# Performance work log

Hardware: AMD Instinct MI355X
Metric: run time of the kernel (lower is better)

## Reference

```python
import jax, jax.numpy as jnp
import numpy as np

B, H, S, D = 4, 16, 4096, 64

def setup_inputs() -> dict:
    key = jax.random.key(0)
    kq, kk, kv, km = jax.random.split(key, 4)
    Q = jax.random.normal(kq, (B, H, S, D), dtype=jnp.float32)
    K = jax.random.normal(kk, (B, H, S, D), dtype=jnp.float32)
    V = jax.random.normal(kv, (B, H, S, D), dtype=jnp.float32)
    mask = jax.random.randint(km, (B, S), 0, 2, dtype=jnp.int32)
    return {"Q": Q, "K": K, "V": V, "mask": mask}

def reference(Q, K, V, mask):
    Q = jax.nn.relu(Q)
    K = jax.nn.relu(K)
    # zero out masked-out key positions: mask [B,S] -> [B,1,S,1]
    m = mask.astype(bool)[:, None, :, None]
    K = jnp.where(m, K, jnp.zeros((), K.dtype))
    # attn_inter = K^T V : [B,H,D,D]
    attn_inter = jnp.einsum('bhsd,bhse->bhde', K, V)
    # attn_weights = Q @ attn_inter : [B,H,S,D]
    attn_weights = jnp.einsum('bhsd,bhde->bhse', Q, attn_inter)
    # norm = Q @ sum_s K : [B,H,S,1]
    k_sum = K.sum(axis=2)  # [B,H,D]
    norm = jnp.einsum('bhsd,bhd->bhs', Q, k_sum)[..., None]
    return attn_weights / norm
```

## Files before the change

### kernel.cpp

```cpp
#include <hip/hip_runtime.h>
#include <hip/hip_bf16.h>

#define SDIM 4096
#define DDIM 64
#define HN   16
#define BH   64
#define NC   16

typedef __attribute__((ext_vector_type(8))) short short8;
typedef __attribute__((ext_vector_type(4))) float f32x4;

static __device__ __forceinline__ unsigned f2bfu(float f) {
    __hip_bfloat16 h = __float2bfloat16(f);
    return (unsigned)*reinterpret_cast<unsigned short*>(&h);
}
static __device__ __forceinline__ short f2bfs(float f) {
    __hip_bfloat16 h = __float2bfloat16(f);
    return *reinterpret_cast<short*>(&h);
}

#define KTPITCH 136

__global__ __launch_bounds__(256, 4) void k1_kv(
    const float* __restrict__ K, const float* __restrict__ V,
    const int* __restrict__ mask,
    float* __restrict__ KVp, float* __restrict__ ksump)
{
    __shared__ __align__(16) char smem[35840];
    char* const KT0 = smem;
    char* const VT0 = smem + 8704;
    char* const KT1 = smem + 17408;
    char* const VT1 = smem + 26112;
    float* const kswork = (float*)(smem + 34816);

    const int tid = threadIdx.x;
    const int w = tid >> 6, l = tid & 63;
    const int a = l & 15, quad = l >> 4;
    const int bh = blockIdx.x >> 4, ch = blockIdx.x & 15;
    const int b  = bh >> 4;
    const long base = (long)bh * SDIM * DDIM;
    const int s0 = ch * 256;

    const int rb  = tid >> 4;
    const int c4  = (tid & 15) << 2;
    const int par = rb & 1;

    f32x4 acc[4];
#pragma unroll
    for (int i = 0; i < 4; ++i) acc[i] = (f32x4){0.f, 0.f, 0.f, 0.f};
    float ks4[4] = {0.f, 0.f, 0.f, 0.f};

    f32x4 kr[4], vr[4];
    float mr[4];
#pragma unroll
    for (int i = 0; i < 4; ++i) {
        const int row = rb + 16 * i;
        kr[i] = *(const f32x4*)(K + base + (long)(s0 + row) * DDIM + c4);
        vr[i] = *(const f32x4*)(V + base + (long)(s0 + row) * DDIM + c4);
        mr[i] = mask[b * SDIM + s0 + row] ? 1.f : 0.f;
    }

    for (int t = 0; t < 4; ++t) {
        char* const KT = (t & 1) ? KT1 : KT0;
        char* const VT = (t & 1) ? VT1 : VT0;

#pragma unroll
        for (int i = 0; i < 4; ++i) {
            const int row = rb + 16 * i;
            const int sp  = row >> 1;
            float kq[4], vq[4];
            kq[0] = fmaxf(kr[i].x, 0.f) * mr[i];
            kq[1] = fmaxf(kr[i].y, 0.f) * mr[i];
            kq[2] = fmaxf(kr[i].z, 0.f) * mr[i];
            kq[3] = fmaxf(kr[i].w, 0.f) * mr[i];
            vq[0] = vr[i].x; vq[1] = vr[i].y; vq[2] = vr[i].z; vq[3] = vr[i].w;
#pragma unroll
            for (int j = 0; j < 4; ++j) ks4[j] += kq[j];
            unsigned ku[4], vu[4];
#pragma unroll
            for (int j = 0; j < 4; ++j) {
                ku[j] = f2bfu(kq[j]);
                vu[j] = f2bfu(vq[j]);
            }
            unsigned kp32[4], vp32[4];
#pragma unroll
            for (int j = 0; j < 4; ++j) {
                const unsigned pk = (unsigned)__shfl_xor((int)ku[j], 16);
                const unsigned pv = (unsigned)__shfl_xor((int)vu[j], 16);
                kp32[j] = par ? (pk | (ku[j] << 16)) : (ku[j] | (pk << 16));
                vp32[j] = par ? (pv | (vu[j] << 16)) : (vu[j] | (pv << 16));
            }
            const int j0 = par * 2;
            *(unsigned*)(KT + (c4 + j0)     * KTPITCH + sp * 4) = kp32[j0];
            *(unsigned*)(KT + (c4 + j0 + 1) * KTPITCH + sp * 4) = kp32[j0 + 1];
            *(unsigned*)(VT + (c4 + j0)     * KTPITCH + sp * 4) = vp32[j0];
            *(unsigned*)(VT + (c4 + j0 + 1) * KTPITCH + sp * 4) = vp32[j0 + 1];
        }

        if (t < 3) {
            const int r0n = s0 + (t + 1) * 64;
#pragma unroll
            for (int i = 0; i < 4; ++i) {
                const int row = rb + 16 * i;
                kr[i] = *(const f32x4*)(K + base + (long)(r0n + row) * DDIM + c4);
                vr[i] = *(const f32x4*)(V + base + (long)(r0n + row) * DDIM + c4);
                mr[i] = mask[b * SDIM + r0n + row] ? 1.f : 0.f;
            }
        }

        __syncthreads();

#pragma unroll
        for (int kh = 0; kh < 2; ++kh) {
            const int sof = kh * 64 + quad * 16;
            short8 af[4];
#pragma unroll
            for (int dt = 0; dt < 4; ++dt) {
                const char* rp = KT + (dt * 16 + a) * KTPITCH + sof;
                const uint2 lo = *(const uint2*)rp;
                const uint2 hi = *(const uint2*)(rp + 8);
                int4 ra; ra.x = lo.x; ra.y = lo.y; ra.z = hi.x; ra.w = hi.y;
                af[dt] = *(short8*)&ra;
            }
            const char* vp = VT + (w * 16 + a) * KTPITCH + sof;
            const uint2 vlo = *(const uint2*)vp;
            const uint2 vhi = *(const uint2*)(vp + 8);
            int4 rb4; rb4.x = vlo.x; rb4.y = vlo.y; rb4.z = vhi.x; rb4.w = vhi.y;
            const short8 bf = *(short8*)&rb4;
#pragma unroll
            for (int dt = 0; dt < 4; ++dt)
                acc[dt] = __builtin_amdgcn_mfma_f32_16x16x32_bf16(
                    af[dt], bf, acc[dt], 0, 0, 0);
        }
    }

#pragma unroll
    for (int j = 0; j < 4; ++j) {
        ks4[j] += __shfl_xor(ks4[j], 16);
        ks4[j] += __shfl_xor(ks4[j], 32);
    }
    __syncthreads();
    float* const kb = (float*)smem;
#pragma unroll
    for (int dt = 0; dt < 4; ++dt)
#pragma unroll
        for (int r = 0; r < 4; ++r) {
            const int d = dt * 16 + quad * 4 + r;
            const int e = w * 16 + a;
            kb[d * 64 + (e ^ (((d >> 3) & 3) << 4))] = acc[dt][r];
        }
    if (l < 16) {
#pragma unroll
        for (int j = 0; j < 4; ++j) kswork[w * 64 + l * 4 + j] = ks4[j];
    }
    __syncthreads();
    float* outp = KVp + ((long)bh * NC + ch) * 4096;
#pragma unroll
    for (int i = 0; i < 16; ++i) {
        const int idx = i * 256 + tid;
        const int d = idx >> 6, e = idx & 63;
        outp[idx] = kb[d * 64 + (e ^ (((d >> 3) & 3) << 4))];
    }
    if (tid < 64)
        ksump[((long)bh * NC + ch) * 64 + tid] =
            kswork[tid] + kswork[64 + tid] + kswork[128 + tid] + kswork[192 + tid];
}

__global__ __launch_bounds__(256) void k2_reduce(
    const float* __restrict__ KVp, const float* __restrict__ ksump,
    float* __restrict__ KV, float* __restrict__ ksum)
{
    const int bh = blockIdx.x >> 2;
    const int qt = blockIdx.x & 3;
    const int tid = threadIdx.x;
#pragma unroll
    for (int i = 0; i < 4; ++i) {
        const int idx = qt * 1024 + i * 256 + tid;
        float v = 0.f;
#pragma unroll
        for (int c = 0; c < NC; ++c) v += KVp[((long)bh * NC + c) * 4096 + idx];
        KV[(long)bh * 4096 + idx] = v;
    }
    if (qt == 0 && tid < 64) {
        float v = 0.f;
#pragma unroll
        for (int c = 0; c < NC; ++c) v += ksump[((long)bh * NC + c) * 64 + tid];
        ksum[bh * 64 + tid] = v;
    }
}

__global__ __launch_bounds__(256, 4) void k3_out(
    const float* __restrict__ Q, const float* __restrict__ KVm,
    const float* __restrict__ ksum, float* __restrict__ out)
{
    __shared__ float cbuf[4][16 * 68];
    const int tid  = threadIdx.x;
    const int w    = tid >> 6;
    const int l    = tid & 63;
    const int r16  = l & 15;
    const int quad = l >> 4;
    const int bh    = blockIdx.x >> 4;
    const int strip = blockIdx.x & 15;

    const float* kvp = KVm + (long)bh * 4096;
    short8 bfrag[2][4];
#pragma unroll
    for (int kh = 0; kh < 2; ++kh)
#pragma unroll
        for (int n = 0; n < 4; ++n) {
            short8 tmp;
#pragma unroll
            for (int j = 0; j < 8; ++j)
                tmp[j] = f2bfs(kvp[(kh * 32 + quad * 8 + j) * 64 + n * 16 + r16]);
            bfrag[kh][n] = tmp;
        }
    float ksv[16];
#pragma unroll
    for (int j = 0; j < 8; ++j) {
        ksv[j]     = ksum[bh * 64 + quad * 8 + j];
        ksv[j + 8] = ksum[bh * 64 + 32 + quad * 8 + j];
    }

    const int rowbase = strip * 256 + w * 64;
    const float* qptr = Q + ((long)bh * SDIM + rowbase + r16) * DDIM + quad * 8;
    float* obase = out + ((long)bh * SDIM + rowbase) * DDIM;
    float* cw = &cbuf[w][0];

    f32x4 a0 = *(const f32x4*)(qptr);
    f32x4 a1 = *(const f32x4*)(qptr + 4);
    f32x4 a2 = *(const f32x4*)(qptr + 32);
    f32x4 a3 = *(const f32x4*)(qptr + 36);

    for (int t = 0; t < 4; ++t) {
        f32x4 b0 = a0, b1 = a1, b2 = a2, b3 = a3;
        if (t < 3) {
            const float* qn = qptr + (t + 1) * 16 * DDIM;
            b0 = *(const f32x4*)(qn);
            b1 = *(const f32x4*)(qn + 4);
            b2 = *(const f32x4*)(qn + 32);
            b3 = *(const f32x4*)(qn + 36);
        }
#pragma unroll
        for (int j = 0; j < 4; ++j) {
            a0[j] = fmaxf(a0[j], 0.f); a1[j] = fmaxf(a1[j], 0.f);
            a2[j] = fmaxf(a2[j], 0.f); a3[j] = fmaxf(a3[j], 0.f);
        }
        float p = 0.f;
#pragma unroll
        for (int j = 0; j < 4; ++j) {
            p = fmaf(a0[j], ksv[j],      p);
            p = fmaf(a1[j], ksv[4 + j],  p);
            p = fmaf(a2[j], ksv[8 + j],  p);
            p = fmaf(a3[j], ksv[12 + j], p);
        }
        p += __shfl_xor(p, 16);
        p += __shfl_xor(p, 32);
        const float inv = __builtin_amdgcn_rcpf(p);

        short8 af0, af1;
#pragma unroll
        for (int j = 0; j < 4; ++j) {
            af0[j]     = f2bfs(a0[j]);
            af0[4 + j] = f2bfs(a1[j]);
            af1[j]     = f2bfs(a2[j]);
            af1[4 + j] = f2bfs(a3[j]);
        }

        f32x4 acc[4];
#pragma unroll
        for (int n = 0; n < 4; ++n) {
            acc[n] = (f32x4){0.f, 0.f, 0.f, 0.f};
            acc[n] = __builtin_amdgcn_mfma_f32_16x16x32_bf16(af0, bfrag[0][n], acc[n], 0, 0, 0);
            acc[n] = __builtin_amdgcn_mfma_f32_16x16x32_bf16(af1, bfrag[1][n], acc[n], 0, 0, 0);
        }

        float invr[4];
#pragma unroll
        for (int r = 0; r < 4; ++r) invr[r] = __shfl(inv, quad * 4 + r);

#pragma unroll
        for (int n = 0; n < 4; ++n)
#pragma unroll
            for (int r = 0; r < 4; ++r)
                cw[(quad * 4 + r) * 68 + n * 16 + r16] = acc[n][r] * invr[r];

        float* ot = obase + (t * 16) * DDIM;
#pragma unroll
        for (int i = 0; i < 4; ++i) {
            f32x4 v = *(const f32x4*)(cw + (i * 4 + quad) * 68 + r16 * 4);
            *(f32x4*)(ot + (i * 4 + quad) * DDIM + r16 * 4) = v;
        }
        a0 = b0; a1 = b1; a2 = b2; a3 = b3;
    }
}

extern "C" void kernel_launch(void* const* d_in, const int* in_sizes, int n_in,
                              void* d_out, int out_size, void* d_ws, size_t ws_size,
                              hipStream_t stream)
{
    const float* Q    = (const float*)d_in[0];
    const float* K    = (const float*)d_in[1];
    const float* V    = (const float*)d_in[2];
    const int*   mask = (const int*)d_in[3];
    float* out = (float*)d_out;

    float* KVp   = out;
    float* ksump = KVp + (long)BH * NC * 4096;
    float* KV    = (float*)d_ws;
    float* ksum  = KV + (long)BH * 4096;

    hipLaunchKernelGGL(k1_kv, dim3(BH * NC), dim3(256), 0, stream,
                       K, V, mask, KVp, ksump);
    hipLaunchKernelGGL(k2_reduce, dim3(BH * 4), dim3(256), 0, stream,
                       KVp, ksump, KV, ksum);
    hipLaunchKernelGGL(k3_out, dim3(BH * 16), dim3(256), 0, stream,
                       Q, KV, ksum, out);
}
```

Before: 67.64 us.

## Split sequence chunk across waves with per-wave full KV tiles and LDS reduction

```diff
diff --git a/kernel.cpp b/kernel.cpp
--- a/kernel.cpp
+++ b/kernel.cpp
@@ -19,120 +19,109 @@
     return *reinterpret_cast<short*>(&h);
 }
 
-#define KTPITCH 136
-
-__global__ __launch_bounds__(256, 4) void k1_kv(
+#define SPITCH 72
+
+__global__ __launch_bounds__(256, 3) void k1_kv(
     const float* __restrict__ K, const float* __restrict__ V,
     const int* __restrict__ mask,
     float* __restrict__ KVp, float* __restrict__ ksump)
 {
-    __shared__ __align__(16) char smem[35840];
-    char* const KT0 = smem;
-    char* const VT0 = smem + 8704;
-    char* const KT1 = smem + 17408;
-    char* const VT1 = smem + 26112;
-    float* const kswork = (float*)(smem + 34816);
-
+    __shared__ __align__(16) char smem[36864];
     const int tid = threadIdx.x;
     const int w = tid >> 6, l = tid & 63;
     const int a = l & 15, quad = l >> 4;
     const int bh = blockIdx.x >> 4, ch = blockIdx.x & 15;
     const int b  = bh >> 4;
     const long base = (long)bh * SDIM * DDIM;
-    const int s0 = ch * 256;
-
-    const int rb  = tid >> 4;
-    const int c4  = (tid & 15) << 2;
-    const int par = rb & 1;
-
-    f32x4 acc[4];
-#pragma unroll
-    for (int i = 0; i < 4; ++i) acc[i] = (f32x4){0.f, 0.f, 0.f, 0.f};
+    const int s0 = ch * 256 + w * 64;
+
+    char* const KT = smem + w * 9216;
+    char* const VT = smem + w * 9216 + 4608;
+    const int par = quad & 1;
+    const int c4  = a << 2;
+
+    f32x4 acc[4][4];
+#pragma unroll
+    for (int i = 0; i < 4; ++i)
+#pragma unroll
+        for (int j = 0; j < 4; ++j) acc[i][j] = (f32x4){0.f, 0.f, 0.f, 0.f};
     float ks4[4] = {0.f, 0.f, 0.f, 0.f};
 
-    f32x4 kr[4], vr[4];
-    float mr[4];
-#pragma unroll
-    for (int i = 0; i < 4; ++i) {
-        const int row = rb + 16 * i;
-        kr[i] = *(const f32x4*)(K + base + (long)(s0 + row) * DDIM + c4);
-        vr[i] = *(const f32x4*)(V + base + (long)(s0 + row) * DDIM + c4);
-        mr[i] = mask[b * SDIM + s0 + row] ? 1.f : 0.f;
-    }
-
-    for (int t = 0; t < 4; ++t) {
-        char* const KT = (t & 1) ? KT1 : KT0;
-        char* const VT = (t & 1) ? VT1 : VT0;
-
-#pragma unroll
-        for (int i = 0; i < 4; ++i) {
-            const int row = rb + 16 * i;
-            const int sp  = row >> 1;
-            float kq[4], vq[4];
-            kq[0] = fmaxf(kr[i].x, 0.f) * mr[i];
-            kq[1] = fmaxf(kr[i].y, 0.f) * mr[i];
-            kq[2] = fmaxf(kr[i].z, 0.f) * mr[i];
-            kq[3] = fmaxf(kr[i].w, 0.f) * mr[i];
-            vq[0] = vr[i].x; vq[1] = vr[i].y; vq[2] = vr[i].z; vq[3] = vr[i].w;
-#pragma unroll
-            for (int j = 0; j < 4; ++j) ks4[j] += kq[j];
+    auto LOADG = [&](int g, f32x4* kr, f32x4* vr, float* mr) {
+#pragma unroll
+        for (int gg = 0; gg < 4; ++gg) {
+            const int row = s0 + g * 16 + gg * 4 + quad;
+            kr[gg] = *(const f32x4*)(K + base + (long)row * DDIM + c4);
+            vr[gg] = *(const f32x4*)(V + base + (long)row * DDIM + c4);
+            mr[gg] = mask[b * SDIM + row] ? 1.f : 0.f;
+        }
+    };
+    auto PACKG = [&](int g, f32x4* kr, f32x4* vr, float* mr) {
+#pragma unroll
+        for (int gg = 0; gg < 4; ++gg) {
+            float kq[4];
+#pragma unroll
+            for (int j = 0; j < 4; ++j) {
+                kq[j] = fmaxf(kr[gg][j], 0.f) * mr[gg];
+                ks4[j] += kq[j];
+            }
             unsigned ku[4], vu[4];
 #pragma unroll
             for (int j = 0; j < 4; ++j) {
                 ku[j] = f2bfu(kq[j]);
-                vu[j] = f2bfu(vq[j]);
+                vu[j] = f2bfu(vr[gg][j]);
             }
-            unsigned kp32[4], vp32[4];
+            const int sp = (g & 1) * 8 + gg * 2 + (quad >> 1);
+            const int j0 = par * 2;
+            unsigned kp[4], vp[4];
 #pragma unroll
             for (int j = 0; j < 4; ++j) {
                 const unsigned pk = (unsigned)__shfl_xor((int)ku[j], 16);
                 const unsigned pv = (unsigned)__shfl_xor((int)vu[j], 16);
-                kp32[j] = par ? (pk | (ku[j] << 16)) : (ku[j] | (pk << 16));
-                vp32[j] = par ? (pv | (vu[j] << 16)) : (vu[j] | (pv << 16));
+                kp[j] = par ? (pk | (ku[j] << 16)) : (ku[j] | (pk << 16));
+                vp[j] = par ? (pv | (vu[j] << 16)) : (vu[j] | (pv << 16));
             }
-            const int j0 = par * 2;
-            *(unsigned*)(KT + (c4 + j0)     * KTPITCH + sp * 4) = kp32[j0];
-            *(unsigned*)(KT + (c4 + j0 + 1) * KTPITCH + sp * 4) = kp32[j0 + 1];
-            *(unsigned*)(VT + (c4 + j0)     * KTPITCH + sp * 4) = vp32[j0];
-            *(unsigned*)(VT + (c4 + j0 + 1) * KTPITCH + sp * 4) = vp32[j0 + 1];
-        }
-
-        if (t < 3) {
-            const int r0n = s0 + (t + 1) * 64;
-#pragma unroll
-            for (int i = 0; i < 4; ++i) {
-                const int row = rb + 16 * i;
-                kr[i] = *(const f32x4*)(K + base + (long)(r0n + row) * DDIM + c4);
-                vr[i] = *(const f32x4*)(V + base + (long)(r0n + row) * DDIM + c4);
-                mr[i] = mask[b * SDIM + r0n + row] ? 1.f : 0.f;
-            }
-        }
-
-        __syncthreads();
-
-#pragma unroll
-        for (int kh = 0; kh < 2; ++kh) {
-            const int sof = kh * 64 + quad * 16;
-            short8 af[4];
-#pragma unroll
-            for (int dt = 0; dt < 4; ++dt) {
-                const char* rp = KT + (dt * 16 + a) * KTPITCH + sof;
-                const uint2 lo = *(const uint2*)rp;
-                const uint2 hi = *(const uint2*)(rp + 8);
-                int4 ra; ra.x = lo.x; ra.y = lo.y; ra.z = hi.x; ra.w = hi.y;
-                af[dt] = *(short8*)&ra;
-            }
-            const char* vp = VT + (w * 16 + a) * KTPITCH + sof;
-            const uint2 vlo = *(const uint2*)vp;
-            const uint2 vhi = *(const uint2*)(vp + 8);
-            int4 rb4; rb4.x = vlo.x; rb4.y = vlo.y; rb4.z = vhi.x; rb4.w = vhi.y;
-            const short8 bf = *(short8*)&rb4;
-#pragma unroll
-            for (int dt = 0; dt < 4; ++dt)
-                acc[dt] = __builtin_amdgcn_mfma_f32_16x16x32_bf16(
-                    af[dt], bf, acc[dt], 0, 0, 0);
-        }
-    }
+            *(unsigned*)(KT + (c4 + j0)     * SPITCH + sp * 4) = kp[j0];
+            *(unsigned*)(KT + (c4 + j0 + 1) * SPITCH + sp * 4) = kp[j0 + 1];
+            *(unsigned*)(VT + (c4 + j0)     * SPITCH + sp * 4) = vp[j0];
+            *(unsigned*)(VT + (c4 + j0 + 1) * SPITCH + sp * 4) = vp[j0 + 1];
+        }
+    };
+    auto COMPUTE = [&]() {
+        short8 af[4], bf[4];
+#pragma unroll
+        for (int dt = 0; dt < 4; ++dt) {
+            const char* rp = KT + (dt * 16 + a) * SPITCH + quad * 16;
+            const uint2 lo = *(const uint2*)rp;
+            const uint2 hi = *(const uint2*)(rp + 8);
+            int4 ra; ra.x = lo.x; ra.y = lo.y; ra.z = hi.x; ra.w = hi.y;
+            af[dt] = *(short8*)&ra;
+            const char* vpn = VT + (dt * 16 + a) * SPITCH + quad * 16;
+            const uint2 vlo = *(const uint2*)vpn;
+            const uint2 vhi = *(const uint2*)(vpn + 8);
+            int4 rb; rb.x = vlo.x; rb.y = vlo.y; rb.z = vhi.x; rb.w = vhi.y;
+            bf[dt] = *(short8*)&rb;
+        }
+#pragma unroll
+        for (int dt = 0; dt < 4; ++dt)
+#pragma unroll
+            for (int et = 0; et < 4; ++et)
+                acc[dt][et] = __builtin_amdgcn_mfma_f32_16x16x32_bf16(
+                    af[dt], bf[et], acc[dt][et], 0, 0, 0);
+    };
+
+    f32x4 kA[4], vA[4], kB[4], vB[4];
+    float mA[4], mB[4];
+    LOADG(0, kA, vA, mA);
+    LOADG(1, kB, vB, mB);
+    PACKG(0, kA, vA, mA);
+    LOADG(2, kA, vA, mA);
+    PACKG(1, kB, vB, mB);
+    LOADG(3, kB, vB, mB);
+    COMPUTE();
+    PACKG(2, kA, vA, mA);
+    PACKG(3, kB, vB, mB);
+    COMPUTE();
 
 #pragma unroll
     for (int j = 0; j < 4; ++j) {
@@ -140,26 +129,30 @@
         ks4[j] += __shfl_xor(ks4[j], 32);
     }
     __syncthreads();
-    float* const kb = (float*)smem;
-#pragma unroll
-    for (int dt = 0; dt < 4; ++dt)
-#pragma unroll
-        for (int r = 0; r < 4; ++r) {
-            const int d = dt * 16 + quad * 4 + r;
-            const int e = w * 16 + a;
-            kb[d * 64 + (e ^ (((d >> 3) & 3) << 4))] = acc[dt][r];
-        }
+    float* const kswork = (float*)(smem + 16384);
     if (l < 16) {
 #pragma unroll
         for (int j = 0; j < 4; ++j) kswork[w * 64 + l * 4 + j] = ks4[j];
     }
-    __syncthreads();
+
+    float* const strip = (float*)smem;
     float* outp = KVp + ((long)bh * NC + ch) * 4096;
 #pragma unroll
-    for (int i = 0; i < 16; ++i) {
-        const int idx = i * 256 + tid;
-        const int d = idx >> 6, e = idx & 63;
-        outp[idx] = kb[d * 64 + (e ^ (((d >> 3) & 3) << 4))];
+    for (int dt = 0; dt < 4; ++dt) {
+        __syncthreads();
+#pragma unroll
+        for (int et = 0; et < 4; ++et)
+#pragma unroll
+            for (int r = 0; r < 4; ++r)
+                strip[w * 1024 + (quad * 4 + r) * 64 + et * 16 + a] =
+                    acc[dt][et][r];
+        __syncthreads();
+#pragma unroll
+        for (int i = 0; i < 4; ++i) {
+            const int idx = i * 256 + tid;
+            outp[dt * 1024 + idx] = strip[idx] + strip[1024 + idx] +
+                                    strip[2048 + idx] + strip[3072 + idx];
+        }
     }
     if (tid < 64)
         ksump[((long)bh * NC + ch) * 64 + tid] =
```

After: 70.04 us. 3.6% more time.
